# Kernel optimization log

Hardware: AMD Instinct MI355X
Metric: run time of the kernel (lower is better)

Reference implementation:

```python
import jax, jax.numpy as jnp
import numpy as np

N_NODES = 50000
N_EDGES = 800000
F_IN, HID, N_CLS = 128, 64, 40
KS = 2  # kernel_size, dim=1, open B-spline, degree=1


def spline_conv(x, src, dst, pseudo, W, root, bias, num_nodes, kernel_size):
    """SplineConv (torch_geometric), dim=1, degree=1, open spline, aggr='mean'."""
    K = kernel_size
    v = pseudo[:, 0] * (K - 1)                       # map [0,1] -> [0, K-1]
    k0 = jnp.clip(jnp.floor(v), 0, K - 2)
    frac = v - k0                                    # linear (degree-1) basis
    i0 = k0.astype(jnp.int32)
    i1 = i0 + 1
    E = src.shape[0]
    e = jnp.arange(E)
    # per-edge kernel coefficients c[e,k] = sum_s basis[e,s]*[idx[e,s]==k]
    c = jnp.zeros((E, K), x.dtype).at[e, i0].add(1.0 - frac).at[e, i1].add(frac)
    xj = x[src]                                      # [E, F_in] gather
    # agg[k] = scatter-add over edges of c[e,k]*xj[e] -> [K, N, F_in]
    agg = jnp.stack([
        jax.ops.segment_sum(c[:, k:k + 1] * xj, dst, num_segments=num_nodes)
        for k in range(K)
    ])
    deg = jax.ops.segment_sum(jnp.ones((E,), x.dtype), dst, num_segments=num_nodes)
    msg = jnp.einsum('kni,kio->no', agg, W) / jnp.maximum(deg, 1.0)[:, None]
    return msg + x @ root + bias


def setup_inputs() -> dict:
    key = jax.random.key(0)
    ks = jax.random.split(key, 9)
    def glorot(k, shape):
        fan_in, fan_out = shape[-2], shape[-1]
        lim = (6.0 / (fan_in + fan_out)) ** 0.5
        return jax.random.uniform(k, shape, jnp.float32, -lim, lim)
    return {
        'x': jax.random.normal(ks[0], (N_NODES, F_IN), jnp.float32),
        'edge_index': jax.random.randint(ks[1], (2, N_EDGES), 0, N_NODES, jnp.int32),
        'edge_attr': jax.random.uniform(ks[2], (N_EDGES, 1), jnp.float32),
        'W1': glorot(ks[3], (KS, F_IN, HID)),
        'root1': glorot(ks[4], (F_IN, HID)),
        'bias1': jnp.zeros((HID,), jnp.float32),
        'W2': glorot(ks[5], (KS, HID, N_CLS)),
        'root2': glorot(ks[6], (HID, N_CLS)),
        'bias2': jnp.zeros((N_CLS,), jnp.float32),
    }


def reference(x, edge_index, edge_attr, W1, root1, bias1, W2, root2, bias2):
    src, dst = edge_index[0], edge_index[1]
    # eval mode: dropout is identity
    h = spline_conv(x, src, dst, edge_attr, W1, root1, bias1, N_NODES, KS)
    h = jax.nn.elu(h)
    out = spline_conv(h, src, dst, edge_attr, W2, root2, bias2, N_NODES, KS)
    return out
```

## Files before the change

### kernel.cpp

```cpp
#include <hip/hip_runtime.h>
#include <math.h>

#define N_NODES 50000
#define N_EDGES 800000
#define F_IN    128
#define HID     64
#define N_CLS   40

#define M1 (3 * HID)
#define K2  192

#define RANGE_SZ 6250
#define PERM_SLICES 128
#define PERM_CHUNK (N_EDGES / PERM_SLICES)
#define EST 64

#define NW (M1 * F_IN + N_CLS * K2)

using sh8 = __attribute__((ext_vector_type(8))) short;
using floatx4 = __attribute__((ext_vector_type(4))) float;

__device__ inline unsigned short f2bf(float f) {
    union { float f; unsigned int u; } c{f};
    unsigned int r = (c.u + 0x7FFF + ((c.u >> 16) & 1)) >> 16;
    return (unsigned short)r;
}
__device__ inline float bf2f(unsigned int u) {
    union { unsigned int u; float f; } c;
    c.u = u << 16;
    return c.f;
}

__global__ void concat_w(const float* __restrict__ W1, const float* __restrict__ root1,
                         const float* __restrict__ W2, const float* __restrict__ root2,
                         unsigned short* __restrict__ WT1, unsigned short* __restrict__ WT2,
                         int* __restrict__ cnt) {
    int i = blockIdx.x * blockDim.x + threadIdx.x;
    if (i < M1 * F_IN) {
        int c = i / F_IN, k = i % F_IN;
        float val;
        if (c < HID)            val = W1[k * HID + c];
        else if (c < 2 * HID)   val = W1[F_IN * HID + k * HID + (c - HID)];
        else                    val = root1[k * HID + (c - 2 * HID)];
        WT1[i] = f2bf(val);
    } else if (i < NW) {
        int ii = i - M1 * F_IN;
        int c = ii / K2, k = ii % K2;
        float val;
        if (k < HID)             val = W2[k * N_CLS + c];
        else if (k < 2 * HID)    val = W2[HID * N_CLS + (k - HID) * N_CLS + c];
        else                     val = root2[(k - 2 * HID) * N_CLS + c];
        WT2[ii] = f2bf(val);
    } else {
        int ii = i - NW;
        if (ii < N_NODES) cnt[ii] = 0;
    }
}

template <int KD, bool AF32, int SPLIT, int PW, int ROOTW, int MT>
__device__ __forceinline__ void gemm_body(int bid, const void* __restrict__ Aptr,
                                          const unsigned short* __restrict__ Bt,
                                          unsigned short* __restrict__ Csp,
                                          float* __restrict__ Croot, int Crows) {
    constexpr int KP = KD + 8;
    __shared__ unsigned short As[64 * KP];
    __shared__ unsigned short Bs[64 * KP];

    int tid = threadIdx.x;
    int row0 = bid * 64;

    if (AF32) {
        const float* A = (const float*)Aptr;
        for (int c = tid; c < 64 * (KD / 4); c += 256) {
            int r = c / (KD / 4), q = c % (KD / 4);
            int gr = row0 + r;
            float4 v = make_float4(0.f, 0.f, 0.f, 0.f);
            if (gr < Crows) v = *(const float4*)(A + (size_t)gr * KD + q * 4);
            union { unsigned short s[4]; uint2 u; } pk;
            pk.s[0] = f2bf(v.x); pk.s[1] = f2bf(v.y);
            pk.s[2] = f2bf(v.z); pk.s[3] = f2bf(v.w);
            *(uint2*)&As[r * KP + q * 4] = pk.u;
        }
    } else {
        const unsigned short* A = (const unsigned short*)Aptr;
        for (int c = tid; c < 64 * (KD / 8); c += 256) {
            int r = c / (KD / 8), q = c % (KD / 8);
            int gr = row0 + r;
            sh8 v = {};
            if (gr < Crows) v = *(const sh8*)(A + (size_t)gr * KD + q * 8);
            *(sh8*)&As[r * KP + q * 8] = v;
        }
    }

    int wv = tid >> 6, lane = tid & 63;
    int lrow = lane & 15, lq = lane >> 4;

    for (int mt = 0; mt < MT; ++mt) {
        int c0 = mt * 64;
        __syncthreads();
        for (int c = tid; c < 64 * (KD / 8); c += 256) {
            int r = c / (KD / 8), q = c % (KD / 8);
            *(sh8*)&Bs[r * KP + q * 8] = *(const sh8*)(Bt + (size_t)(c0 + r) * KD + q * 8);
        }
        __syncthreads();

        floatx4 acc[4] = {{0.f,0.f,0.f,0.f},{0.f,0.f,0.f,0.f},{0.f,0.f,0.f,0.f},{0.f,0.f,0.f,0.f}};
#pragma unroll
        for (int kt = 0; kt < KD / 32; ++kt) {
            int kb = kt * 32 + lq * 8;
            sh8 a0 = *(const sh8*)&As[(wv * 16 + lrow) * KP + kb];
#pragma unroll
            for (int cf = 0; cf < 4; ++cf) {
                sh8 b = *(const sh8*)&Bs[(cf * 16 + lrow) * KP + kb];
                acc[cf] = __builtin_amdgcn_mfma_f32_16x16x32_bf16(a0, b, acc[cf], 0, 0, 0);
            }
        }

#pragma unroll
        for (int r = 0; r < 4; ++r) {
            int gr = row0 + wv * 16 + lq * 4 + r;
            if (gr >= Crows) continue;
#pragma unroll
            for (int cf = 0; cf < 4; ++cf) {
                int gc = c0 + cf * 16 + lrow;
                float val = acc[cf][r];
                if (gc < SPLIT) {
                    int pi = (gc < PW) ? gc * 2 : (gc - PW) * 2 + 1;
                    Csp[(size_t)gr * SPLIT + pi] = f2bf(val);
                } else if (gc < SPLIT + ROOTW) {
                    Croot[(size_t)gr * ROOTW + (gc - SPLIT)] = val;
                }
            }
        }
    }
}

__device__ __forceinline__ void permute_body(int b, const int* __restrict__ src,
                                             const int* __restrict__ dst,
                                             const float* __restrict__ attr,
                                             int* __restrict__ cnt,
                                             unsigned int* __restrict__ edata) {
    int range = b & 7;
    int slice = b >> 3;
    int lo = range * RANGE_SZ;
    int e0 = slice * PERM_CHUNK;
    int e1 = e0 + PERM_CHUNK;
    for (int e = e0 + (int)threadIdx.x; e < e1; e += 256) {
        int d = dst[e];
        if ((unsigned)(d - lo) < (unsigned)RANGE_SZ) {
            int pos = atomicAdd(&cnt[d], 1);
            if (pos < EST) {
                unsigned int q = (unsigned int)(attr[e] * 65535.0f + 0.5f);
                edata[d * EST + pos] = (unsigned int)src[e] | (q << 16);
            }
        }
    }
}

__global__ __launch_bounds__(256) void gemm1_permute(const float* __restrict__ x,
                                                     const unsigned short* __restrict__ WT1,
                                                     unsigned short* __restrict__ Ysp,
                                                     float* __restrict__ Yroot,
                                                     const int* __restrict__ src,
                                                     const int* __restrict__ dst,
                                                     const float* __restrict__ attr,
                                                     int* __restrict__ cnt,
                                                     unsigned int* __restrict__ edata,
                                                     int gemmBlocks) {
    if ((int)blockIdx.x < gemmBlocks) {
        gemm_body<128, true, 128, 64, 64, 3>(blockIdx.x, (const void*)x, WT1, Ysp, Yroot, N_NODES);
    } else {
        permute_body(blockIdx.x - gemmBlocks, src, dst, attr, cnt, edata);
    }
}

__global__ __launch_bounds__(256) void gather1(const unsigned short* __restrict__ Ysp,
                                               const float* __restrict__ Yroot,
                                               const int* __restrict__ cnt,
                                               const unsigned int* __restrict__ edata,
                                               const float* __restrict__ bias1,
                                               unsigned short* __restrict__ h,
                                               unsigned short* __restrict__ A192) {
    int wave = (blockIdx.x * blockDim.x + threadIdx.x) >> 6;
    int lane = threadIdx.x & 63;
    if (wave >= N_NODES) return;
    int hf = lane >> 5;
    int c  = lane & 31;
    int deg = cnt[wave];
    deg = deg > EST ? EST : deg;
    const unsigned int* eb = edata + (size_t)wave * EST;
    const float qs = 1.0f / 65535.0f;
    float a0 = 0.0f, a1 = 0.0f;
    if (deg <= 16) {
        unsigned int e[8]; uint2 p[8];
#pragma unroll
        for (int t = 0; t < 8; ++t) e[t] = eb[2 * t + hf];
#pragma unroll
        for (int t = 0; t < 8; ++t) {
            int idx = (2 * t + hf < deg) ? (int)(e[t] & 0xffffu) : 0;
            p[t] = *(const uint2*)(Ysp + (size_t)idx * 128 + c * 4);
        }
#pragma unroll
        for (int t = 0; t < 8; ++t) {
            float m = (2 * t + hf < deg) ? 1.0f : 0.0f;
            float v = (float)(e[t] >> 16) * qs;
            float w = 1.0f - v;
            a0 += m * (w * bf2f(p[t].x & 0xffffu) + v * bf2f(p[t].x >> 16));
            a1 += m * (w * bf2f(p[t].y & 0xffffu) + v * bf2f(p[t].y >> 16));
        }
    } else {
        unsigned int e[16]; uint2 p[16];
#pragma unroll
        for (int t = 0; t < 16; ++t) e[t] = eb[2 * t + hf];
#pragma unroll
        for (int t = 0; t < 16; ++t) {
            int idx = (2 * t + hf < deg) ? (int)(e[t] & 0xffffu) : 0;
            p[t] = *(const uint2*)(Ysp + (size_t)idx * 128 + c * 4);
        }
#pragma unroll
        for (int t = 0; t < 16; ++t) {
            float m = (2 * t + hf < deg) ? 1.0f : 0.0f;
            float v = (float)(e[t] >> 16) * qs;
            float w = 1.0f - v;
            a0 += m * (w * bf2f(p[t].x & 0xffffu) + v * bf2f(p[t].x >> 16));
            a1 += m * (w * bf2f(p[t].y & 0xffffu) + v * bf2f(p[t].y >> 16));
        }
        if (deg > 32) {
            for (int j = 32 + hf; j < deg; j += 2) {
                unsigned int ee = eb[j];
                int idx = (int)(ee & 0xffffu);
                uint2 pp = *(const uint2*)(Ysp + (size_t)idx * 128 + c * 4);
                float v = (float)(ee >> 16) * qs;
                float w = 1.0f - v;
                a0 += w * bf2f(pp.x & 0xffffu) + v * bf2f(pp.x >> 16);
                a1 += w * bf2f(pp.y & 0xffffu) + v * bf2f(pp.y >> 16);
            }
        }
    }
    a0 += __shfl_xor(a0, 32);
    a1 += __shfl_xor(a1, 32);
    float dg = (float)deg;
    dg = dg > 1.0f ? dg : 1.0f;
    float2 yr = *(const float2*)(Yroot + (size_t)wave * HID + c * 2);
    float2 bi = *(const float2*)(bias1 + c * 2);
    float m0 = a0 / dg + yr.x + bi.x;
    float m1 = a1 / dg + yr.y + bi.y;
    m0 = m0 > 0.0f ? m0 : expm1f(m0);
    m1 = m1 > 0.0f ? m1 : expm1f(m1);
    if (hf == 0) {
        unsigned int u = (unsigned int)f2bf(m0) | ((unsigned int)f2bf(m1) << 16);
        *(unsigned int*)(h + (size_t)wave * HID + c * 2) = u;
        *(unsigned int*)(A192 + (size_t)wave * K2 + 128 + c * 2) = u;
    }
}

__global__ __launch_bounds__(256) void gather2h(const unsigned short* __restrict__ hb,
                                                const int* __restrict__ cnt,
                                                const unsigned int* __restrict__ edata,
                                                unsigned short* __restrict__ A192) {
    int wave = (blockIdx.x * blockDim.x + threadIdx.x) >> 6;
    int lane = threadIdx.x & 63;
    if (wave >= N_NODES) return;
    int hf = lane >> 5;
    int c  = lane & 31;
    int deg = cnt[wave];
    deg = deg > EST ? EST : deg;
    const unsigned int* eb = edata + (size_t)wave * EST;
    const float qs = 1.0f / 65535.0f;
    float a00 = 0.0f, a01 = 0.0f, a10 = 0.0f, a11 = 0.0f;
    if (deg <= 16) {
        unsigned int e[8], p[8];
#pragma unroll
        for (int t = 0; t < 8; ++t) e[t] = eb[2 * t + hf];
#pragma unroll
        for (int t = 0; t < 8; ++t) {
            int idx = (2 * t + hf < deg) ? (int)(e[t] & 0xffffu) : 0;
            p[t] = *(const unsigned int*)(hb + (size_t)idx * HID + c * 2);
        }
#pragma unroll
        for (int t = 0; t < 8; ++t) {
            float m = (2 * t + hf < deg) ? 1.0f : 0.0f;
            float v = (float)(e[t] >> 16) * qs;
            float wm = m * (1.0f - v), vm = m * v;
            float h0 = bf2f(p[t] & 0xffffu), h1 = bf2f(p[t] >> 16);
            a00 += wm * h0; a01 += wm * h1;
            a10 += vm * h0; a11 += vm * h1;
        }
    } else {
        unsigned int e[16], p[16];
#pragma unroll
        for (int t = 0; t < 16; ++t) e[t] = eb[2 * t + hf];
#pragma unroll
        for (int t = 0; t < 16; ++t) {
            int idx = (2 * t + hf < deg) ? (int)(e[t] & 0xffffu) : 0;
            p[t] = *(const unsigned int*)(hb + (size_t)idx * HID + c * 2);
        }
#pragma unroll
        for (int t = 0; t < 16; ++t) {
            float m = (2 * t + hf < deg) ? 1.0f : 0.0f;
            float v = (float)(e[t] >> 16) * qs;
            float wm = m * (1.0f - v), vm = m * v;
            float h0 = bf2f(p[t] & 0xffffu), h1 = bf2f(p[t] >> 16);
            a00 += wm * h0; a01 += wm * h1;
            a10 += vm * h0; a11 += vm * h1;
        }
        if (deg > 32) {
            for (int j = 32 + hf; j < deg; j += 2) {
                unsigned int ee = eb[j];
                int idx = (int)(ee & 0xffffu);
                unsigned int pp = *(const unsigned int*)(hb + (size_t)idx * HID + c * 2);
                float v = (float)(ee >> 16) * qs;
                float w = 1.0f - v;
                float h0 = bf2f(pp & 0xffffu), h1 = bf2f(pp >> 16);
                a00 += w * h0; a01 += w * h1;
                a10 += v * h0; a11 += v * h1;
            }
        }
    }
    a00 += __shfl_xor(a00, 32);
    a01 += __shfl_xor(a01, 32);
    a10 += __shfl_xor(a10, 32);
    a11 += __shfl_xor(a11, 32);
    if (hf == 0) {
        float dg = (float)deg;
        dg = dg > 1.0f ? dg : 1.0f;
        float inv = 1.0f / dg;
        unsigned int u0 = (unsigned int)f2bf(a00 * inv) | ((unsigned int)f2bf(a01 * inv) << 16);
        unsigned int u1 = (unsigned int)f2bf(a10 * inv) | ((unsigned int)f2bf(a11 * inv) << 16);
        *(unsigned int*)(A192 + (size_t)wave * K2 + c * 2) = u0;
        *(unsigned int*)(A192 + (size_t)wave * K2 + 64 + c * 2) = u1;
    }
}

__global__ __launch_bounds__(256) void gemm_out(const unsigned short* __restrict__ A,
                                                const unsigned short* __restrict__ Bt,
                                                const float* __restrict__ bias2,
                                                float* __restrict__ out) {
    constexpr int KD = K2, KP = KD + 8;
    __shared__ unsigned short As[64 * KP];
    __shared__ unsigned short Bs[64 * KP];

    int tid = threadIdx.x;
    int row0 = blockIdx.x * 64;

    for (int c = tid; c < 64 * (KD / 8); c += 256) {
        int r = c / (KD / 8), q = c % (KD / 8);
        int gr = row0 + r;
        sh8 v = {};
        if (gr < N_NODES) v = *(const sh8*)(A + (size_t)gr * KD + q * 8);
        *(sh8*)&As[r * KP + q * 8] = v;
    }
    for (int c = tid; c < 64 * (KD / 8); c += 256) {
        int r = c / (KD / 8), q = c % (KD / 8);
        sh8 v = {};
        if (r < N_CLS) v = *(const sh8*)(Bt + (size_t)r * KD + q * 8);
        *(sh8*)&Bs[r * KP + q * 8] = v;
    }
    __syncthreads();

    int wv = tid >> 6, lane = tid & 63;
    int lrow = lane & 15, lq = lane >> 4;

    floatx4 acc[4] = {{0.f,0.f,0.f,0.f},{0.f,0.f,0.f,0.f},{0.f,0.f,0.f,0.f},{0.f,0.f,0.f,0.f}};
#pragma unroll
    for (int kt = 0; kt < KD / 32; ++kt) {
        int kb = kt * 32 + lq * 8;
        sh8 a0 = *(const sh8*)&As[(wv * 16 + lrow) * KP + kb];
#pragma unroll
        for (int cf = 0; cf < 4; ++cf) {
            sh8 b = *(const sh8*)&Bs[(cf * 16 + lrow) * KP + kb];
            acc[cf] = __builtin_amdgcn_mfma_f32_16x16x32_bf16(a0, b, acc[cf], 0, 0, 0);
        }
    }

#pragma unroll
    for (int r = 0; r < 4; ++r) {
        int gr = row0 + wv * 16 + lq * 4 + r;
        if (gr >= N_NODES) continue;
#pragma unroll
        for (int cf = 0; cf < 4; ++cf) {
            int gc = cf * 16 + lrow;
            if (gc < N_CLS) {
                out[(size_t)gr * N_CLS + gc] = acc[cf][r] + bias2[gc];
            }
        }
    }
}

extern "C" void kernel_launch(void* const* d_in, const int* in_sizes, int n_in,
                              void* d_out, int out_size, void* d_ws, size_t ws_size,
                              hipStream_t stream) {
    const float* x     = (const float*)d_in[0];
    const int*   eidx  = (const int*)d_in[1];
    const float* eattr = (const float*)d_in[2];
    const float* W1    = (const float*)d_in[3];
    const float* root1 = (const float*)d_in[4];
    const float* bias1 = (const float*)d_in[5];
    const float* W2    = (const float*)d_in[6];
    const float* root2 = (const float*)d_in[7];
    const float* bias2 = (const float*)d_in[8];
    float* out = (float*)d_out;

    const int* src = eidx;
    const int* dst = eidx + N_EDGES;

    char* base = (char*)d_ws;
    unsigned short* Ysp   = (unsigned short*)base;
    float*          Yroot = (float*)(base + 12800000);
    unsigned short* hb    = (unsigned short*)(base + 25600000);
    unsigned short* WT1   = (unsigned short*)(base + 32000000);
    unsigned short* WT2   = (unsigned short*)(base + 32049152);
    unsigned int*   edata = (unsigned int*)(base + 32065536);
    int*            cnt   = (int*)(base + 44865536);
    unsigned short* A192  = (unsigned short*)(base + 45065536);

    const int GB = (N_NODES + 63) / 64;

    hipLaunchKernelGGL(concat_w, dim3((NW + N_NODES + 255) / 256), dim3(256), 0, stream,
                       W1, root1, W2, root2, WT1, WT2, cnt);

    hipLaunchKernelGGL(gemm1_permute, dim3(GB + 8 * PERM_SLICES), dim3(256), 0, stream,
                       x, WT1, Ysp, Yroot, src, dst, eattr, cnt, edata, GB);

    hipLaunchKernelGGL(gather1, dim3((N_NODES * 64 + 255) / 256), dim3(256), 0, stream,
                       Ysp, Yroot, cnt, edata, bias1, hb, A192);

    hipLaunchKernelGGL(gather2h, dim3((N_NODES * 64 + 255) / 256), dim3(256), 0, stream,
                       hb, cnt, edata, A192);

    hipLaunchKernelGGL(gemm_out, dim3(GB), dim3(256), 0, stream,
                       A192, WT2, bias2, out);
}
```

Measured before the change: 198.2 us.

## Fuse layer-2 neighbor gather into output GEMM via shared-memory A tile

Merges gather2h and gemm_out into one kernel. Each block gathers its 64 nodes' aggregated features into LDS and then runs MFMA directly against WT2 read from global memory, which is padded to 64 rows with zeros. This removes the A192 round trip through global memory and one kernel launch. In exchange, the gather parallelism drops to 782 blocks with each wave handling 16 nodes serially, so latency hiding in the gather may be worse.

```diff
diff --git a/kernel.cpp b/kernel.cpp
--- a/kernel.cpp
+++ b/kernel.cpp
@@ -9,13 +9,14 @@
 
 #define M1 (3 * HID)
 #define K2  192
+#define C2P 64
 
 #define RANGE_SZ 6250
 #define PERM_SLICES 128
 #define PERM_CHUNK (N_EDGES / PERM_SLICES)
 #define EST 64
 
-#define NW (M1 * F_IN + N_CLS * K2)
+#define NW (M1 * F_IN + C2P * K2)
 
 using sh8 = __attribute__((ext_vector_type(8))) short;
 using floatx4 = __attribute__((ext_vector_type(4))) float;
@@ -46,10 +47,12 @@
     } else if (i < NW) {
         int ii = i - M1 * F_IN;
         int c = ii / K2, k = ii % K2;
-        float val;
-        if (k < HID)             val = W2[k * N_CLS + c];
-        else if (k < 2 * HID)    val = W2[HID * N_CLS + (k - HID) * N_CLS + c];
-        else                     val = root2[(k - 2 * HID) * N_CLS + c];
+        float val = 0.0f;
+        if (c < N_CLS) {
+            if (k < HID)             val = W2[k * N_CLS + c];
+            else if (k < 2 * HID)    val = W2[HID * N_CLS + (k - HID) * N_CLS + c];
+            else                     val = root2[(k - 2 * HID) * N_CLS + c];
+        }
         WT2[ii] = f2bf(val);
     } else {
         int ii = i - NW;
@@ -179,8 +182,7 @@
                                                const int* __restrict__ cnt,
                                                const unsigned int* __restrict__ edata,
                                                const float* __restrict__ bias1,
-                                               unsigned short* __restrict__ h,
-                                               unsigned short* __restrict__ A192) {
+                                               unsigned short* __restrict__ h) {
     int wave = (blockIdx.x * blockDim.x + threadIdx.x) >> 6;
     int lane = threadIdx.x & 63;
     if (wave >= N_NODES) return;
@@ -250,125 +252,119 @@
     if (hf == 0) {
         unsigned int u = (unsigned int)f2bf(m0) | ((unsigned int)f2bf(m1) << 16);
         *(unsigned int*)(h + (size_t)wave * HID + c * 2) = u;
-        *(unsigned int*)(A192 + (size_t)wave * K2 + 128 + c * 2) = u;
-    }
-}
-
-__global__ __launch_bounds__(256) void gather2h(const unsigned short* __restrict__ hb,
-                                                const int* __restrict__ cnt,
-                                                const unsigned int* __restrict__ edata,
-                                                unsigned short* __restrict__ A192) {
-    int wave = (blockIdx.x * blockDim.x + threadIdx.x) >> 6;
-    int lane = threadIdx.x & 63;
-    if (wave >= N_NODES) return;
-    int hf = lane >> 5;
-    int c  = lane & 31;
-    int deg = cnt[wave];
-    deg = deg > EST ? EST : deg;
-    const unsigned int* eb = edata + (size_t)wave * EST;
-    const float qs = 1.0f / 65535.0f;
-    float a00 = 0.0f, a01 = 0.0f, a10 = 0.0f, a11 = 0.0f;
-    if (deg <= 16) {
-        unsigned int e[8], p[8];
-#pragma unroll
-        for (int t = 0; t < 8; ++t) e[t] = eb[2 * t + hf];
-#pragma unroll
-        for (int t = 0; t < 8; ++t) {
-            int idx = (2 * t + hf < deg) ? (int)(e[t] & 0xffffu) : 0;
-            p[t] = *(const unsigned int*)(hb + (size_t)idx * HID + c * 2);
-        }
-#pragma unroll
-        for (int t = 0; t < 8; ++t) {
-            float m = (2 * t + hf < deg) ? 1.0f : 0.0f;
-            float v = (float)(e[t] >> 16) * qs;
-            float wm = m * (1.0f - v), vm = m * v;
-            float h0 = bf2f(p[t] & 0xffffu), h1 = bf2f(p[t] >> 16);
-            a00 += wm * h0; a01 += wm * h1;
-            a10 += vm * h0; a11 += vm * h1;
-        }
-    } else {
-        unsigned int e[16], p[16];
-#pragma unroll
-        for (int t = 0; t < 16; ++t) e[t] = eb[2 * t + hf];
-#pragma unroll
-        for (int t = 0; t < 16; ++t) {
-            int idx = (2 * t + hf < deg) ? (int)(e[t] & 0xffffu) : 0;
-            p[t] = *(const unsigned int*)(hb + (size_t)idx * HID + c * 2);
-        }
-#pragma unroll
-        for (int t = 0; t < 16; ++t) {
-            float m = (2 * t + hf < deg) ? 1.0f : 0.0f;
-            float v = (float)(e[t] >> 16) * qs;
-            float wm = m * (1.0f - v), vm = m * v;
-            float h0 = bf2f(p[t] & 0xffffu), h1 = bf2f(p[t] >> 16);
-            a00 += wm * h0; a01 += wm * h1;
-            a10 += vm * h0; a11 += vm * h1;
-        }
-        if (deg > 32) {
-            for (int j = 32 + hf; j < deg; j += 2) {
-                unsigned int ee = eb[j];
-                int idx = (int)(ee & 0xffffu);
-                unsigned int pp = *(const unsigned int*)(hb + (size_t)idx * HID + c * 2);
-                float v = (float)(ee >> 16) * qs;
-                float w = 1.0f - v;
-                float h0 = bf2f(pp & 0xffffu), h1 = bf2f(pp >> 16);
-                a00 += w * h0; a01 += w * h1;
-                a10 += v * h0; a11 += v * h1;
-            }
-        }
-    }
-    a00 += __shfl_xor(a00, 32);
-    a01 += __shfl_xor(a01, 32);
-    a10 += __shfl_xor(a10, 32);
-    a11 += __shfl_xor(a11, 32);
-    if (hf == 0) {
-        float dg = (float)deg;
-        dg = dg > 1.0f ? dg : 1.0f;
-        float inv = 1.0f / dg;
-        unsigned int u0 = (unsigned int)f2bf(a00 * inv) | ((unsigned int)f2bf(a01 * inv) << 16);
-        unsigned int u1 = (unsigned int)f2bf(a10 * inv) | ((unsigned int)f2bf(a11 * inv) << 16);
-        *(unsigned int*)(A192 + (size_t)wave * K2 + c * 2) = u0;
-        *(unsigned int*)(A192 + (size_t)wave * K2 + 64 + c * 2) = u1;
-    }
-}
-
-__global__ __launch_bounds__(256) void gemm_out(const unsigned short* __restrict__ A,
-                                                const unsigned short* __restrict__ Bt,
-                                                const float* __restrict__ bias2,
-                                                float* __restrict__ out) {
-    constexpr int KD = K2, KP = KD + 8;
-    __shared__ unsigned short As[64 * KP];
-    __shared__ unsigned short Bs[64 * KP];
-
+    }
+}
+
+__global__ __launch_bounds__(256) void g2gemm(const unsigned short* __restrict__ hb,
+                                              const int* __restrict__ cnt,
+                                              const unsigned int* __restrict__ edata,
+                                              const unsigned short* __restrict__ WT2,
+                                              const float* __restrict__ bias2,
+                                              float* __restrict__ out) {
+    constexpr int AP = 200;
+    __shared__ unsigned short As[64 * AP];
     int tid = threadIdx.x;
     int row0 = blockIdx.x * 64;
-
-    for (int c = tid; c < 64 * (KD / 8); c += 256) {
-        int r = c / (KD / 8), q = c % (KD / 8);
-        int gr = row0 + r;
-        sh8 v = {};
-        if (gr < N_NODES) v = *(const sh8*)(A + (size_t)gr * KD + q * 8);
-        *(sh8*)&As[r * KP + q * 8] = v;
-    }
-    for (int c = tid; c < 64 * (KD / 8); c += 256) {
-        int r = c / (KD / 8), q = c % (KD / 8);
-        sh8 v = {};
-        if (r < N_CLS) v = *(const sh8*)(Bt + (size_t)r * KD + q * 8);
-        *(sh8*)&Bs[r * KP + q * 8] = v;
+    int wv = tid >> 6, lane = tid & 63;
+    int hf = lane >> 5, c = lane & 31;
+    const float qs = 1.0f / 65535.0f;
+
+    for (int i = 0; i < 16; ++i) {
+        int arow = wv * 16 + i;
+        int node = row0 + arow;
+        float a00 = 0.0f, a01 = 0.0f, a10 = 0.0f, a11 = 0.0f;
+        int deg = 0;
+        if (node < N_NODES) {
+            deg = cnt[node];
+            deg = deg > EST ? EST : deg;
+            const unsigned int* eb = edata + (size_t)node * EST;
+            if (deg <= 16) {
+                unsigned int e[8], p[8];
+#pragma unroll
+                for (int t = 0; t < 8; ++t) e[t] = eb[2 * t + hf];
+#pragma unroll
+                for (int t = 0; t < 8; ++t) {
+                    int idx = (2 * t + hf < deg) ? (int)(e[t] & 0xffffu) : 0;
+                    p[t] = *(const unsigned int*)(hb + (size_t)idx * HID + c * 2);
+                }
+#pragma unroll
+                for (int t = 0; t < 8; ++t) {
+                    float m = (2 * t + hf < deg) ? 1.0f : 0.0f;
+                    float v = (float)(e[t] >> 16) * qs;
+                    float wm = m * (1.0f - v), vm = m * v;
+                    float h0 = bf2f(p[t] & 0xffffu), h1 = bf2f(p[t] >> 16);
+                    a00 += wm * h0; a01 += wm * h1;
+                    a10 += vm * h0; a11 += vm * h1;
+                }
+            } else {
+                unsigned int e[16], p[16];
+#pragma unroll
+                for (int t = 0; t < 16; ++t) e[t] = eb[2 * t + hf];
+#pragma unroll
+                for (int t = 0; t < 16; ++t) {
+                    int idx = (2 * t + hf < deg) ? (int)(e[t] & 0xffffu) : 0;
+                    p[t] = *(const unsigned int*)(hb + (size_t)idx * HID + c * 2);
+                }
+#pragma unroll
+                for (int t = 0; t < 16; ++t) {
+                    float m = (2 * t + hf < deg) ? 1.0f : 0.0f;
+                    float v = (float)(e[t] >> 16) * qs;
+                    float wm = m * (1.0f - v), vm = m * v;
+                    float h0 = bf2f(p[t] & 0xffffu), h1 = bf2f(p[t] >> 16);
+                    a00 += wm * h0; a01 += wm * h1;
+                    a10 += vm * h0; a11 += vm * h1;
+                }
+                if (deg > 32) {
+                    for (int j = 32 + hf; j < deg; j += 2) {
+                        unsigned int ee = eb[j];
+                        int idx = (int)(ee & 0xffffu);
+                        unsigned int pp = *(const unsigned int*)(hb + (size_t)idx * HID + c * 2);
+                        float v = (float)(ee >> 16) * qs;
+                        float w = 1.0f - v;
+                        float h0 = bf2f(pp & 0xffffu), h1 = bf2f(pp >> 16);
+                        a00 += w * h0; a01 += w * h1;
+                        a10 += v * h0; a11 += v * h1;
+                    }
+                }
+            }
+        }
+        a00 += __shfl_xor(a00, 32);
+        a01 += __shfl_xor(a01, 32);
+        a10 += __shfl_xor(a10, 32);
+        a11 += __shfl_xor(a11, 32);
+        if (node < N_NODES) {
+            if (hf == 0) {
+                float dg = (float)deg;
+                dg = dg > 1.0f ? dg : 1.0f;
+                float inv = 1.0f / dg;
+                unsigned int u0 = (unsigned int)f2bf(a00 * inv) | ((unsigned int)f2bf(a01 * inv) << 16);
+                unsigned int u1 = (unsigned int)f2bf(a10 * inv) | ((unsigned int)f2bf(a11 * inv) << 16);
+                *(unsigned int*)&As[arow * AP + c * 2] = u0;
+                *(unsigned int*)&As[arow * AP + 64 + c * 2] = u1;
+            } else {
+                unsigned int u = *(const unsigned int*)(hb + (size_t)node * HID + c * 2);
+                *(unsigned int*)&As[arow * AP + 128 + c * 2] = u;
+            }
+        } else {
+            if (hf == 0) {
+                *(unsigned int*)&As[arow * AP + c * 2] = 0u;
+                *(unsigned int*)&As[arow * AP + 64 + c * 2] = 0u;
+            } else {
+                *(unsigned int*)&As[arow * AP + 128 + c * 2] = 0u;
+            }
+        }
     }
     __syncthreads();
 
-    int wv = tid >> 6, lane = tid & 63;
     int lrow = lane & 15, lq = lane >> 4;
-
     floatx4 acc[4] = {{0.f,0.f,0.f,0.f},{0.f,0.f,0.f,0.f},{0.f,0.f,0.f,0.f},{0.f,0.f,0.f,0.f}};
 #pragma unroll
-    for (int kt = 0; kt < KD / 32; ++kt) {
+    for (int kt = 0; kt < K2 / 32; ++kt) {
         int kb = kt * 32 + lq * 8;
-        sh8 a0 = *(const sh8*)&As[(wv * 16 + lrow) * KP + kb];
+        sh8 a0 = *(const sh8*)&As[(wv * 16 + lrow) * AP + kb];
 #pragma unroll
         for (int cf = 0; cf < 4; ++cf) {
-            sh8 b = *(const sh8*)&Bs[(cf * 16 + lrow) * KP + kb];
+            sh8 b = *(const sh8*)(WT2 + (size_t)(cf * 16 + lrow) * K2 + kb);
             acc[cf] = __builtin_amdgcn_mfma_f32_16x16x32_bf16(a0, b, acc[cf], 0, 0, 0);
         }
     }
@@ -410,9 +406,8 @@
     unsigned short* hb    = (unsigned short*)(base + 25600000);
     unsigned short* WT1   = (unsigned short*)(base + 32000000);
     unsigned short* WT2   = (unsigned short*)(base + 32049152);
-    unsigned int*   edata = (unsigned int*)(base + 32065536);
-    int*            cnt   = (int*)(base + 44865536);
-    unsigned short* A192  = (unsigned short*)(base + 45065536);
+    unsigned int*   edata = (unsigned int*)(base + 32073728);
+    int*            cnt   = (int*)(base + 44873728);
 
     const int GB = (N_NODES + 63) / 64;
 
@@ -423,11 +418,8 @@
                        x, WT1, Ysp, Yroot, src, dst, eattr, cnt, edata, GB);
 
     hipLaunchKernelGGL(gather1, dim3((N_NODES * 64 + 255) / 256), dim3(256), 0, stream,
-                       Ysp, Yroot, cnt, edata, bias1, hb, A192);
-
-    hipLaunchKernelGGL(gather2h, dim3((N_NODES * 64 + 255) / 256), dim3(256), 0, stream,
-                       hb, cnt, edata, A192);
-
-    hipLaunchKernelGGL(gemm_out, dim3(GB), dim3(256), 0, stream,
-                       A192, WT2, bias2, out);
-}
+                       Ysp, Yroot, cnt, edata, bias1, hb);
+
+    hipLaunchKernelGGL(g2gemm, dim3(GB), dim3(256), 0, stream,
+                       hb, cnt, edata, WT2, bias2, out);
+}
```

Result: slower. 209.2 us (+5.5%).

## Reorder layer-1 as aggregate-then-transform and merge preprocessing into one prep kernel

Applied to the files above, without the earlier changes.

Layer 1 now gathers bf16 x rows per edge into two spline-weighted 128-wide aggregates, then runs one K=384 GEMM with bias and ELU fused. Before, it ran the GEMM first and gathered the 128-wide transformed features. The edge permutation no longer scans the edges once per node range; each slice scatters all its edges directly with batched atomics, and x-to-bf16 casting and weight packing share one prep kernel. The GEMMs read B straight from global memory instead of staging it in LDS. In exchange there is more gather traffic per edge (128 bf16 instead of 128 packed values, roughly the same), extra Agg round-trip memory, and atomics with far more contention because the range filtering is gone.

```diff
diff --git a/kernel.cpp b/kernel.cpp
--- a/kernel.cpp
+++ b/kernel.cpp
@@ -7,15 +7,20 @@
 #define HID     64
 #define N_CLS   40
 
-#define M1 (3 * HID)
-#define K2  192
-
-#define RANGE_SZ 6250
+#define K1 384
+#define K2 192
+#define C1 64
+#define C2P 64
+
 #define PERM_SLICES 128
 #define PERM_CHUNK (N_EDGES / PERM_SLICES)
 #define EST 64
 
-#define NW (M1 * F_IN + N_CLS * K2)
+#define NW1 (C1 * K1)
+#define NW2 (C2P * K2)
+#define NWT (NW1 + NW2)
+#define CONCAT_BLOCKS (NWT / 256)
+#define XCAST_BLOCKS 3125
 
 using sh8 = __attribute__((ext_vector_type(8))) short;
 using floatx4 = __attribute__((ext_vector_type(4))) float;
@@ -29,110 +34,6 @@
     union { unsigned int u; float f; } c;
     c.u = u << 16;
     return c.f;
-}
-
-__global__ void concat_w(const float* __restrict__ W1, const float* __restrict__ root1,
-                         const float* __restrict__ W2, const float* __restrict__ root2,
-                         unsigned short* __restrict__ WT1, unsigned short* __restrict__ WT2,
-                         int* __restrict__ cnt) {
-    int i = blockIdx.x * blockDim.x + threadIdx.x;
-    if (i < M1 * F_IN) {
-        int c = i / F_IN, k = i % F_IN;
-        float val;
-        if (c < HID)            val = W1[k * HID + c];
-        else if (c < 2 * HID)   val = W1[F_IN * HID + k * HID + (c - HID)];
-        else                    val = root1[k * HID + (c - 2 * HID)];
-        WT1[i] = f2bf(val);
-    } else if (i < NW) {
-        int ii = i - M1 * F_IN;
-        int c = ii / K2, k = ii % K2;
-        float val;
-        if (k < HID)             val = W2[k * N_CLS + c];
-        else if (k < 2 * HID)    val = W2[HID * N_CLS + (k - HID) * N_CLS + c];
-        else                     val = root2[(k - 2 * HID) * N_CLS + c];
-        WT2[ii] = f2bf(val);
-    } else {
-        int ii = i - NW;
-        if (ii < N_NODES) cnt[ii] = 0;
-    }
-}
-
-template <int KD, bool AF32, int SPLIT, int PW, int ROOTW, int MT>
-__device__ __forceinline__ void gemm_body(int bid, const void* __restrict__ Aptr,
-                                          const unsigned short* __restrict__ Bt,
-                                          unsigned short* __restrict__ Csp,
-                                          float* __restrict__ Croot, int Crows) {
-    constexpr int KP = KD + 8;
-    __shared__ unsigned short As[64 * KP];
-    __shared__ unsigned short Bs[64 * KP];
-
-    int tid = threadIdx.x;
-    int row0 = bid * 64;
-
-    if (AF32) {
-        const float* A = (const float*)Aptr;
-        for (int c = tid; c < 64 * (KD / 4); c += 256) {
-            int r = c / (KD / 4), q = c % (KD / 4);
-            int gr = row0 + r;
-            float4 v = make_float4(0.f, 0.f, 0.f, 0.f);
-            if (gr < Crows) v = *(const float4*)(A + (size_t)gr * KD + q * 4);
-            union { unsigned short s[4]; uint2 u; } pk;
-            pk.s[0] = f2bf(v.x); pk.s[1] = f2bf(v.y);
-            pk.s[2] = f2bf(v.z); pk.s[3] = f2bf(v.w);
-            *(uint2*)&As[r * KP + q * 4] = pk.u;
-        }
-    } else {
-        const unsigned short* A = (const unsigned short*)Aptr;
-        for (int c = tid; c < 64 * (KD / 8); c += 256) {
-            int r = c / (KD / 8), q = c % (KD / 8);
-            int gr = row0 + r;
-            sh8 v = {};
-            if (gr < Crows) v = *(const sh8*)(A + (size_t)gr * KD + q * 8);
-            *(sh8*)&As[r * KP + q * 8] = v;
-        }
-    }
-
-    int wv = tid >> 6, lane = tid & 63;
-    int lrow = lane & 15, lq = lane >> 4;
-
-    for (int mt = 0; mt < MT; ++mt) {
-        int c0 = mt * 64;
-        __syncthreads();
-        for (int c = tid; c < 64 * (KD / 8); c += 256) {
-            int r = c / (KD / 8), q = c % (KD / 8);
-            *(sh8*)&Bs[r * KP + q * 8] = *(const sh8*)(Bt + (size_t)(c0 + r) * KD + q * 8);
-        }
-        __syncthreads();
-
-        floatx4 acc[4] = {{0.f,0.f,0.f,0.f},{0.f,0.f,0.f,0.f},{0.f,0.f,0.f,0.f},{0.f,0.f,0.f,0.f}};
-#pragma unroll
-        for (int kt = 0; kt < KD / 32; ++kt) {
-            int kb = kt * 32 + lq * 8;
-            sh8 a0 = *(const sh8*)&As[(wv * 16 + lrow) * KP + kb];
-#pragma unroll
-            for (int cf = 0; cf < 4; ++cf) {
-                sh8 b = *(const sh8*)&Bs[(cf * 16 + lrow) * KP + kb];
-                acc[cf] = __builtin_amdgcn_mfma_f32_16x16x32_bf16(a0, b, acc[cf], 0, 0, 0);
-            }
-        }
-
-#pragma unroll
-        for (int r = 0; r < 4; ++r) {
-            int gr = row0 + wv * 16 + lq * 4 + r;
-            if (gr >= Crows) continue;
-#pragma unroll
-            for (int cf = 0; cf < 4; ++cf) {
-                int gc = c0 + cf * 16 + lrow;
-                float val = acc[cf][r];
-                if (gc < SPLIT) {
-                    int pi = (gc < PW) ? gc * 2 : (gc - PW) * 2 + 1;
-                    Csp[(size_t)gr * SPLIT + pi] = f2bf(val);
-                } else if (gc < SPLIT + ROOTW) {
-                    Croot[(size_t)gr * ROOTW + (gc - SPLIT)] = val;
-                }
-            }
-        }
-    }
 }
 
 __device__ __forceinline__ void permute_body(int b, const int* __restrict__ src,
@@ -140,124 +41,182 @@
                                              const float* __restrict__ attr,
                                              int* __restrict__ cnt,
                                              unsigned int* __restrict__ edata) {
-    int range = b & 7;
-    int slice = b >> 3;
-    int lo = range * RANGE_SZ;
-    int e0 = slice * PERM_CHUNK;
+    int e0 = b * PERM_CHUNK;
     int e1 = e0 + PERM_CHUNK;
-    for (int e = e0 + (int)threadIdx.x; e < e1; e += 256) {
-        int d = dst[e];
-        if ((unsigned)(d - lo) < (unsigned)RANGE_SZ) {
-            int pos = atomicAdd(&cnt[d], 1);
-            if (pos < EST) {
+    for (int base = e0 + (int)threadIdx.x; base < e1; base += 256 * 8) {
+        int d[8];
+        unsigned int pay[8];
+        int pos[8];
+#pragma unroll
+        for (int t = 0; t < 8; ++t) {
+            int e = base + t * 256;
+            d[t] = (e < e1) ? dst[e] : -1;
+        }
+#pragma unroll
+        for (int t = 0; t < 8; ++t) {
+            int e = base + t * 256;
+            pay[t] = 0u;
+            if (d[t] >= 0) {
                 unsigned int q = (unsigned int)(attr[e] * 65535.0f + 0.5f);
-                edata[d * EST + pos] = (unsigned int)src[e] | (q << 16);
+                pay[t] = (unsigned int)src[e] | (q << 16);
             }
         }
-    }
-}
-
-__global__ __launch_bounds__(256) void gemm1_permute(const float* __restrict__ x,
-                                                     const unsigned short* __restrict__ WT1,
-                                                     unsigned short* __restrict__ Ysp,
-                                                     float* __restrict__ Yroot,
-                                                     const int* __restrict__ src,
-                                                     const int* __restrict__ dst,
-                                                     const float* __restrict__ attr,
-                                                     int* __restrict__ cnt,
-                                                     unsigned int* __restrict__ edata,
-                                                     int gemmBlocks) {
-    if ((int)blockIdx.x < gemmBlocks) {
-        gemm_body<128, true, 128, 64, 64, 3>(blockIdx.x, (const void*)x, WT1, Ysp, Yroot, N_NODES);
+#pragma unroll
+        for (int t = 0; t < 8; ++t) {
+            pos[t] = (d[t] >= 0) ? atomicAdd(&cnt[d[t]], 1) : 0;
+        }
+#pragma unroll
+        for (int t = 0; t < 8; ++t) {
+            if (d[t] >= 0 && pos[t] < EST) edata[d[t] * EST + pos[t]] = pay[t];
+        }
+    }
+}
+
+__global__ __launch_bounds__(256) void prep(const int* __restrict__ src,
+                                            const int* __restrict__ dst,
+                                            const float* __restrict__ attr,
+                                            const float* __restrict__ W1,
+                                            const float* __restrict__ root1,
+                                            const float* __restrict__ W2,
+                                            const float* __restrict__ root2,
+                                            const float* __restrict__ x,
+                                            int* __restrict__ cnt,
+                                            unsigned int* __restrict__ edata,
+                                            unsigned short* __restrict__ WT1,
+                                            unsigned short* __restrict__ WT2,
+                                            unsigned short* __restrict__ xb) {
+    int b = blockIdx.x;
+    if (b < PERM_SLICES) {
+        permute_body(b, src, dst, attr, cnt, edata);
+    } else if (b < PERM_SLICES + CONCAT_BLOCKS) {
+        int i = (b - PERM_SLICES) * 256 + (int)threadIdx.x;
+        if (i < NW1) {
+            int c = i / K1, k = i % K1;
+            float val;
+            if (k < 128)       val = W1[k * HID + c];
+            else if (k < 256)  val = W1[F_IN * HID + (k - 128) * HID + c];
+            else               val = root1[(k - 256) * HID + c];
+            WT1[i] = f2bf(val);
+        } else {
+            int ii = i - NW1;
+            int c = ii / K2, k = ii % K2;
+            float val = 0.0f;
+            if (c < N_CLS) {
+                if (k < HID)            val = W2[k * N_CLS + c];
+                else if (k < 2 * HID)   val = W2[HID * N_CLS + (k - HID) * N_CLS + c];
+                else                    val = root2[(k - 2 * HID) * N_CLS + c];
+            }
+            WT2[ii] = f2bf(val);
+        }
     } else {
-        permute_body(blockIdx.x - gemmBlocks, src, dst, attr, cnt, edata);
-    }
-}
-
-__global__ __launch_bounds__(256) void gather1(const unsigned short* __restrict__ Ysp,
-                                               const float* __restrict__ Yroot,
+        int j = (b - PERM_SLICES - CONCAT_BLOCKS) * 256 + (int)threadIdx.x;
+        if (j < 800000) {
+            const float4* xs = (const float4*)x;
+            float4 v0 = xs[j * 2], v1 = xs[j * 2 + 1];
+            union { unsigned short s[8]; sh8 v; } pk;
+            pk.s[0] = f2bf(v0.x); pk.s[1] = f2bf(v0.y);
+            pk.s[2] = f2bf(v0.z); pk.s[3] = f2bf(v0.w);
+            pk.s[4] = f2bf(v1.x); pk.s[5] = f2bf(v1.y);
+            pk.s[6] = f2bf(v1.z); pk.s[7] = f2bf(v1.w);
+            *(sh8*)(xb + (size_t)j * 8) = pk.v;
+        }
+    }
+}
+
+__global__ __launch_bounds__(256) void gatherX(const unsigned short* __restrict__ xb,
                                                const int* __restrict__ cnt,
                                                const unsigned int* __restrict__ edata,
-                                               const float* __restrict__ bias1,
-                                               unsigned short* __restrict__ h,
-                                               unsigned short* __restrict__ A192) {
+                                               unsigned short* __restrict__ Agg) {
     int wave = (blockIdx.x * blockDim.x + threadIdx.x) >> 6;
     int lane = threadIdx.x & 63;
     if (wave >= N_NODES) return;
-    int hf = lane >> 5;
-    int c  = lane & 31;
     int deg = cnt[wave];
     deg = deg > EST ? EST : deg;
     const unsigned int* eb = edata + (size_t)wave * EST;
     const float qs = 1.0f / 65535.0f;
-    float a0 = 0.0f, a1 = 0.0f;
-    if (deg <= 16) {
-        unsigned int e[8]; uint2 p[8];
-#pragma unroll
-        for (int t = 0; t < 8; ++t) e[t] = eb[2 * t + hf];
-#pragma unroll
-        for (int t = 0; t < 8; ++t) {
-            int idx = (2 * t + hf < deg) ? (int)(e[t] & 0xffffu) : 0;
-            p[t] = *(const uint2*)(Ysp + (size_t)idx * 128 + c * 4);
-        }
-#pragma unroll
-        for (int t = 0; t < 8; ++t) {
-            float m = (2 * t + hf < deg) ? 1.0f : 0.0f;
+    float aw0 = 0.0f, aw1 = 0.0f, av0 = 0.0f, av1 = 0.0f;
+    for (int done = 0; done < deg; done += 16) {
+        unsigned int e[16], p[16];
+#pragma unroll
+        for (int t = 0; t < 16; ++t) e[t] = eb[done + t];
+#pragma unroll
+        for (int t = 0; t < 16; ++t) {
+            int idx = (done + t < deg) ? (int)(e[t] & 0xffffu) : 0;
+            p[t] = *(const unsigned int*)(xb + (size_t)idx * F_IN + lane * 2);
+        }
+#pragma unroll
+        for (int t = 0; t < 16; ++t) {
+            float m = (done + t < deg) ? 1.0f : 0.0f;
             float v = (float)(e[t] >> 16) * qs;
-            float w = 1.0f - v;
-            a0 += m * (w * bf2f(p[t].x & 0xffffu) + v * bf2f(p[t].x >> 16));
-            a1 += m * (w * bf2f(p[t].y & 0xffffu) + v * bf2f(p[t].y >> 16));
-        }
-    } else {
-        unsigned int e[16]; uint2 p[16];
-#pragma unroll
-        for (int t = 0; t < 16; ++t) e[t] = eb[2 * t + hf];
-#pragma unroll
-        for (int t = 0; t < 16; ++t) {
-            int idx = (2 * t + hf < deg) ? (int)(e[t] & 0xffffu) : 0;
-            p[t] = *(const uint2*)(Ysp + (size_t)idx * 128 + c * 4);
-        }
-#pragma unroll
-        for (int t = 0; t < 16; ++t) {
-            float m = (2 * t + hf < deg) ? 1.0f : 0.0f;
-            float v = (float)(e[t] >> 16) * qs;
-            float w = 1.0f - v;
-            a0 += m * (w * bf2f(p[t].x & 0xffffu) + v * bf2f(p[t].x >> 16));
-            a1 += m * (w * bf2f(p[t].y & 0xffffu) + v * bf2f(p[t].y >> 16));
-        }
-        if (deg > 32) {
-            for (int j = 32 + hf; j < deg; j += 2) {
-                unsigned int ee = eb[j];
-                int idx = (int)(ee & 0xffffu);
-                uint2 pp = *(const uint2*)(Ysp + (size_t)idx * 128 + c * 4);
-                float v = (float)(ee >> 16) * qs;
-                float w = 1.0f - v;
-                a0 += w * bf2f(pp.x & 0xffffu) + v * bf2f(pp.x >> 16);
-                a1 += w * bf2f(pp.y & 0xffffu) + v * bf2f(pp.y >> 16);
-            }
-        }
-    }
-    a0 += __shfl_xor(a0, 32);
-    a1 += __shfl_xor(a1, 32);
+            float w = m * (1.0f - v);
+            v *= m;
+            float x0 = bf2f(p[t] & 0xffffu), x1 = bf2f(p[t] >> 16);
+            aw0 += w * x0; aw1 += w * x1;
+            av0 += v * x0; av1 += v * x1;
+        }
+    }
     float dg = (float)deg;
     dg = dg > 1.0f ? dg : 1.0f;
-    float2 yr = *(const float2*)(Yroot + (size_t)wave * HID + c * 2);
-    float2 bi = *(const float2*)(bias1 + c * 2);
-    float m0 = a0 / dg + yr.x + bi.x;
-    float m1 = a1 / dg + yr.y + bi.y;
-    m0 = m0 > 0.0f ? m0 : expm1f(m0);
-    m1 = m1 > 0.0f ? m1 : expm1f(m1);
-    if (hf == 0) {
-        unsigned int u = (unsigned int)f2bf(m0) | ((unsigned int)f2bf(m1) << 16);
-        *(unsigned int*)(h + (size_t)wave * HID + c * 2) = u;
-        *(unsigned int*)(A192 + (size_t)wave * K2 + 128 + c * 2) = u;
+    float inv = 1.0f / dg;
+    unsigned int u0 = (unsigned int)f2bf(aw0 * inv) | ((unsigned int)f2bf(aw1 * inv) << 16);
+    unsigned int u1 = (unsigned int)f2bf(av0 * inv) | ((unsigned int)f2bf(av1 * inv) << 16);
+    *(unsigned int*)(Agg + (size_t)wave * 256 + lane * 2) = u0;
+    *(unsigned int*)(Agg + (size_t)wave * 256 + 128 + lane * 2) = u1;
+}
+
+__global__ __launch_bounds__(256) void gemm1h(const unsigned short* __restrict__ Agg,
+                                              const unsigned short* __restrict__ xb,
+                                              const unsigned short* __restrict__ WT1,
+                                              const float* __restrict__ bias1,
+                                              unsigned short* __restrict__ hb) {
+    constexpr int KD = K1, KP = KD + 8;
+    __shared__ unsigned short As[64 * KP];
+    int tid = threadIdx.x;
+    int row0 = blockIdx.x * 64;
+
+    for (int cidx = tid; cidx < 64 * (KD / 8); cidx += 256) {
+        int r = cidx / (KD / 8), q = cidx % (KD / 8);
+        int gr = row0 + r;
+        sh8 v = {};
+        if (gr < N_NODES) {
+            if (q < 32) v = *(const sh8*)(Agg + (size_t)gr * 256 + q * 8);
+            else        v = *(const sh8*)(xb + (size_t)gr * 128 + (q - 32) * 8);
+        }
+        *(sh8*)&As[r * KP + q * 8] = v;
+    }
+    __syncthreads();
+
+    int wv = tid >> 6, lane = tid & 63;
+    int lrow = lane & 15, lq = lane >> 4;
+    floatx4 acc[4] = {{0.f,0.f,0.f,0.f},{0.f,0.f,0.f,0.f},{0.f,0.f,0.f,0.f},{0.f,0.f,0.f,0.f}};
+#pragma unroll
+    for (int kt = 0; kt < KD / 32; ++kt) {
+        int kb = kt * 32 + lq * 8;
+        sh8 a0 = *(const sh8*)&As[(wv * 16 + lrow) * KP + kb];
+#pragma unroll
+        for (int cf = 0; cf < 4; ++cf) {
+            sh8 b = *(const sh8*)(WT1 + (size_t)(cf * 16 + lrow) * KD + kb);
+            acc[cf] = __builtin_amdgcn_mfma_f32_16x16x32_bf16(a0, b, acc[cf], 0, 0, 0);
+        }
+    }
+#pragma unroll
+    for (int r = 0; r < 4; ++r) {
+        int gr = row0 + wv * 16 + lq * 4 + r;
+        if (gr >= N_NODES) continue;
+#pragma unroll
+        for (int cf = 0; cf < 4; ++cf) {
+            int gc = cf * 16 + lrow;
+            float m = acc[cf][r] + bias1[gc];
+            m = m > 0.0f ? m : expm1f(m);
+            hb[(size_t)gr * HID + gc] = f2bf(m);
+        }
     }
 }
 
 __global__ __launch_bounds__(256) void gather2h(const unsigned short* __restrict__ hb,
                                                 const int* __restrict__ cnt,
                                                 const unsigned int* __restrict__ edata,
-                                                unsigned short* __restrict__ A192) {
+                                                unsigned short* __restrict__ A128) {
     int wave = (blockIdx.x * blockDim.x + threadIdx.x) >> 6;
     int lane = threadIdx.x & 63;
     if (wave >= N_NODES) return;
@@ -327,40 +286,35 @@
         float inv = 1.0f / dg;
         unsigned int u0 = (unsigned int)f2bf(a00 * inv) | ((unsigned int)f2bf(a01 * inv) << 16);
         unsigned int u1 = (unsigned int)f2bf(a10 * inv) | ((unsigned int)f2bf(a11 * inv) << 16);
-        *(unsigned int*)(A192 + (size_t)wave * K2 + c * 2) = u0;
-        *(unsigned int*)(A192 + (size_t)wave * K2 + 64 + c * 2) = u1;
-    }
-}
-
-__global__ __launch_bounds__(256) void gemm_out(const unsigned short* __restrict__ A,
-                                                const unsigned short* __restrict__ Bt,
+        *(unsigned int*)(A128 + (size_t)wave * 128 + c * 2) = u0;
+        *(unsigned int*)(A128 + (size_t)wave * 128 + 64 + c * 2) = u1;
+    }
+}
+
+__global__ __launch_bounds__(256) void gemm_out(const unsigned short* __restrict__ A128,
+                                                const unsigned short* __restrict__ hb,
+                                                const unsigned short* __restrict__ WT2,
                                                 const float* __restrict__ bias2,
                                                 float* __restrict__ out) {
     constexpr int KD = K2, KP = KD + 8;
     __shared__ unsigned short As[64 * KP];
-    __shared__ unsigned short Bs[64 * KP];
-
     int tid = threadIdx.x;
     int row0 = blockIdx.x * 64;
 
-    for (int c = tid; c < 64 * (KD / 8); c += 256) {
-        int r = c / (KD / 8), q = c % (KD / 8);
+    for (int cidx = tid; cidx < 64 * (KD / 8); cidx += 256) {
+        int r = cidx / (KD / 8), q = cidx % (KD / 8);
         int gr = row0 + r;
         sh8 v = {};
-        if (gr < N_NODES) v = *(const sh8*)(A + (size_t)gr * KD + q * 8);
+        if (gr < N_NODES) {
+            if (q < 16) v = *(const sh8*)(A128 + (size_t)gr * 128 + q * 8);
+            else        v = *(const sh8*)(hb + (size_t)gr * 64 + (q - 16) * 8);
+        }
         *(sh8*)&As[r * KP + q * 8] = v;
-    }
-    for (int c = tid; c < 64 * (KD / 8); c += 256) {
-        int r = c / (KD / 8), q = c % (KD / 8);
-        sh8 v = {};
-        if (r < N_CLS) v = *(const sh8*)(Bt + (size_t)r * KD + q * 8);
-        *(sh8*)&Bs[r * KP + q * 8] = v;
     }
     __syncthreads();
 
     int wv = tid >> 6, lane = tid & 63;
     int lrow = lane & 15, lq = lane >> 4;
-
     floatx4 acc[4] = {{0.f,0.f,0.f,0.f},{0.f,0.f,0.f,0.f},{0.f,0.f,0.f,0.f},{0.f,0.f,0.f,0.f}};
 #pragma unroll
     for (int kt = 0; kt < KD / 32; ++kt) {
@@ -368,11 +322,10 @@
         sh8 a0 = *(const sh8*)&As[(wv * 16 + lrow) * KP + kb];
 #pragma unroll
         for (int cf = 0; cf < 4; ++cf) {
-            sh8 b = *(const sh8*)&Bs[(cf * 16 + lrow) * KP + kb];
+            sh8 b = *(const sh8*)(WT2 + (size_t)(cf * 16 + lrow) * KD + kb);
             acc[cf] = __builtin_amdgcn_mfma_f32_16x16x32_bf16(a0, b, acc[cf], 0, 0, 0);
         }
     }
-
 #pragma unroll
     for (int r = 0; r < 4; ++r) {
         int gr = row0 + wv * 16 + lq * 4 + r;
@@ -405,29 +358,30 @@
     const int* dst = eidx + N_EDGES;
 
     char* base = (char*)d_ws;
-    unsigned short* Ysp   = (unsigned short*)base;
-    float*          Yroot = (float*)(base + 12800000);
-    unsigned short* hb    = (unsigned short*)(base + 25600000);
-    unsigned short* WT1   = (unsigned short*)(base + 32000000);
-    unsigned short* WT2   = (unsigned short*)(base + 32049152);
-    unsigned int*   edata = (unsigned int*)(base + 32065536);
-    int*            cnt   = (int*)(base + 44865536);
-    unsigned short* A192  = (unsigned short*)(base + 45065536);
+    unsigned short* xb    = (unsigned short*)base;
+    unsigned short* Agg   = (unsigned short*)(base + 12800000);
+    unsigned short* hb    = (unsigned short*)(base + 38400000);
+    unsigned short* A128  = (unsigned short*)(base + 44800000);
+    unsigned short* WT1   = (unsigned short*)(base + 57600000);
+    unsigned short* WT2   = (unsigned short*)(base + 57649152);
+    unsigned int*   edata = (unsigned int*)(base + 57673728);
+    int*            cnt   = (int*)(base + 70473728);
 
     const int GB = (N_NODES + 63) / 64;
 
-    hipLaunchKernelGGL(concat_w, dim3((NW + N_NODES + 255) / 256), dim3(256), 0, stream,
-                       W1, root1, W2, root2, WT1, WT2, cnt);
-
-    hipLaunchKernelGGL(gemm1_permute, dim3(GB + 8 * PERM_SLICES), dim3(256), 0, stream,
-                       x, WT1, Ysp, Yroot, src, dst, eattr, cnt, edata, GB);
-
-    hipLaunchKernelGGL(gather1, dim3((N_NODES * 64 + 255) / 256), dim3(256), 0, stream,
-                       Ysp, Yroot, cnt, edata, bias1, hb, A192);
+    hipMemsetAsync(cnt, 0, N_NODES * sizeof(int), stream);
+    hipLaunchKernelGGL(prep, dim3(PERM_SLICES + CONCAT_BLOCKS + XCAST_BLOCKS), dim3(256), 0, stream,
+                       src, dst, eattr, W1, root1, W2, root2, x, cnt, edata, WT1, WT2, xb);
+
+    hipLaunchKernelGGL(gatherX, dim3((N_NODES * 64 + 255) / 256), dim3(256), 0, stream,
+                       xb, cnt, edata, Agg);
+
+    hipLaunchKernelGGL(gemm1h, dim3(GB), dim3(256), 0, stream,
+                       Agg, xb, WT1, bias1, hb);
 
     hipLaunchKernelGGL(gather2h, dim3((N_NODES * 64 + 255) / 256), dim3(256), 0, stream,
-                       hb, cnt, edata, A192);
+                       hb, cnt, edata, A128);
 
     hipLaunchKernelGGL(gemm_out, dim3(GB), dim3(256), 0, stream,
-                       A192, WT2, bias2, out);
-}
+                       A128, hb, WT2, bias2, out);
+}
```

Result: slower. 243.5 us (+22.8%).
